# Kernel tuning notes

Measured on AMD Instinct MI355X. Metric: run time of the kernel, lower is better.

Reference implementation:

```python
import jax, jax.numpy as jnp
import numpy as np

# Dims / scalars (from init_kwargs: m = int(T/dt), delta = dt, theta_star = threshold)
M = 50000
N = 500
DELTA = 0.001
GLEAK = 1.0
TAUS = 10.0
THETA_STAR = 1.0
SPIKE_PROB = 0.02  # sparse binary spike raster as produced by time2spike


def setup_inputs() -> dict:
    key = jax.random.key(0)
    k1, k2, k3 = jax.random.split(key, 3)
    # binary spike raster [m, n]
    spikes = (jax.random.uniform(k1, (M, N)) < SPIKE_PROB).astype(jnp.float32)
    # synapse weights ~ N(w_mean=0.01, 0.01)
    w = (0.01 + 0.01 * jax.random.normal(k2, (N,))).astype(jnp.float32)
    # reversal potentials: half excitatory (ex=5), half inhibitory (inh=-1), shuffled
    vrev = jnp.where(jax.random.uniform(k3, (N,)) < 0.5, 5.0, -1.0).astype(jnp.float32)
    return {"spikes": spikes, "w": w, "vrev": vrev}


def reference(spikes, w, vrev):
    dtype = spikes.dtype
    decay = jnp.exp(jnp.asarray(-1.0 / TAUS, dtype))

    # _compute_exp: exp_temp[i] = (exp_temp[i-1] + spikes[i-1]) * exp(-1/taus), exp_temp[0] = 0
    def exp_step(carry, s):
        nxt = (carry + s) * decay
        return nxt, nxt

    _, e_tail = jax.lax.scan(exp_step, jnp.zeros((N,), dtype), spikes[:-1])
    exp_temp = jnp.concatenate([jnp.zeros((1, N), dtype), e_tail], axis=0)  # [M, N]

    # Gsyn_pre = |w| * exp_temp ; Isyn_pre = Vrev * |w| * exp_temp.
    # Only their per-timestep sums over synapses enter the vtr recurrence,
    # so contract over n immediately instead of materializing [M, N] products.
    absw = jnp.abs(w)
    g_sum = exp_temp @ absw            # [M] = sum_j Gsyn_pre[i, j]
    i_sum = exp_temp @ (vrev * absw)   # [M] = sum_j Isyn_pre[i, j]
    a = DELTA * (GLEAK + g_sum)        # per-step leak+conductance factor
    b = DELTA * i_sum                  # per-step input drive

    # _computevtr: if vtr[i-1] < theta: vtr[i] = vtr[i-1]*(1 - a[i-1]) + b[i-1]
    # else vtr[i] stays 0 (state reset after threshold crossing), vtr[0] = 0.
    def vtr_step(v, ab):
        ai, bi = ab
        nxt = jnp.where(v < THETA_STAR, v * (1.0 - ai) + bi, jnp.asarray(0.0, dtype))
        return nxt, nxt

    _, v_tail = jax.lax.scan(vtr_step, jnp.asarray(0.0, dtype), (a[:-1], b[:-1]))
    vtr = jnp.concatenate([jnp.zeros((1,), dtype), v_tail])  # [M]
    return vtr
```

## Files before the change

### kernel.cpp

```cpp
#include <hip/hip_runtime.h>
#include <cmath>

namespace {
constexpr int NELEM  = 50000;
constexpr int NSYN   = 500;
constexpr int NQ4    = 125;
constexpr int T      = 1024;
constexpr int SBLK   = 49;
constexpr int SLOTS  = SBLK * T;
constexpr int CMAXC  = (NELEM - 1) >> 6;
constexpr int NCH_PAD = 784;
constexpr int MAXSEG = 4096;
constexpr int NGRP   = NELEM / 8;
constexpr double DELTA_D = 1.0e-3;
constexpr double THETA_D = 1.0;
constexpr float  DECAY_F = 0.90483741803595957311f;
}

struct WS {
    double2 pq[SLOTS];
    double  rarr[SLOTS];
    double  qarr[SLOTS];
    double  eAm[SLOTS], eAg[SLOTS], eAi[SLOTS];
    double  ePl[SLOTS], eQl[SLOTS];
    double  gAm[64], gAg[64], gAi[64];
    double  gPp[64], gPq[64];
    double  gmaxR[1024];
    double  gbndQ[MAXSEG];
    int     gbnd[MAXSEG];
    int     gnseg;
    int     pad;
    float   swv[SLOTS];
    float   iwv[SLOTS];
};

__global__ __launch_bounds__(256) void k_rowdot(
    const float* __restrict__ spikes,
    const float* __restrict__ w,
    const float* __restrict__ vrev,
    float* __restrict__ swv,
    float* __restrict__ iwv)
{
    const int lane = threadIdx.x & 63;
    const int wv   = threadIdx.x >> 6;
    const int rg   = blockIdx.x * 4 + wv;
    if (rg >= NGRP) return;
    const int row0 = rg * 8;

    const float4* __restrict__ w4 = reinterpret_cast<const float4*>(w);
    const float4* __restrict__ r4 = reinterpret_cast<const float4*>(vrev);
    const int j1 = lane;
    const int j2 = lane + 64;
    const bool has2 = (j2 < NQ4);
    float4 a1 = w4[j1], r1 = r4[j1];
    float4 aw1 = make_float4(fabsf(a1.x), fabsf(a1.y), fabsf(a1.z), fabsf(a1.w));
    float4 ar1 = make_float4(aw1.x * r1.x, aw1.y * r1.y, aw1.z * r1.z, aw1.w * r1.w);
    float4 aw2 = make_float4(0.f, 0.f, 0.f, 0.f), ar2 = aw2;
    if (has2) {
        float4 a2 = w4[j2], r2 = r4[j2];
        aw2 = make_float4(fabsf(a2.x), fabsf(a2.y), fabsf(a2.z), fabsf(a2.w));
        ar2 = make_float4(aw2.x * r2.x, aw2.y * r2.y, aw2.z * r2.z, aw2.w * r2.w);
    }

    float4 s1[8], s2[8];
#pragma unroll
    for (int r = 0; r < 8; ++r) {
        const float4* __restrict__ srow =
            reinterpret_cast<const float4*>(spikes + (size_t)(row0 + r) * NSYN);
        s1[r] = srow[j1];
        if (has2) s2[r] = srow[j2];
    }
    float sp[8], ip[8];
#pragma unroll
    for (int r = 0; r < 8; ++r) {
        float a = s1[r].x * aw1.x + s1[r].y * aw1.y + s1[r].z * aw1.z + s1[r].w * aw1.w;
        float b = s1[r].x * ar1.x + s1[r].y * ar1.y + s1[r].z * ar1.z + s1[r].w * ar1.w;
        if (has2) {
            a += s2[r].x * aw2.x + s2[r].y * aw2.y + s2[r].z * aw2.z + s2[r].w * aw2.w;
            b += s2[r].x * ar2.x + s2[r].y * ar2.y + s2[r].z * ar2.z + s2[r].w * ar2.w;
        }
        sp[r] = a; ip[r] = b;
    }
#pragma unroll
    for (int d = 32; d > 0; d >>= 1) {
#pragma unroll
        for (int r = 0; r < 8; ++r) {
            sp[r] += __shfl_xor(sp[r], d);
            ip[r] += __shfl_xor(ip[r], d);
        }
    }
    if (lane == 0) {
        *reinterpret_cast<float4*>(swv + row0)     = make_float4(sp[0], sp[1], sp[2], sp[3]);
        *reinterpret_cast<float4*>(swv + row0 + 4) = make_float4(sp[4], sp[5], sp[6], sp[7]);
        *reinterpret_cast<float4*>(iwv + row0)     = make_float4(ip[0], ip[1], ip[2], ip[3]);
        *reinterpret_cast<float4*>(iwv + row0 + 4) = make_float4(ip[4], ip[5], ip[6], ip[7]);
    }
}

__global__ __launch_bounds__(1024) void k_scanA(WS* __restrict__ ws)
{
    const int tid = threadIdx.x, lane = tid & 63, wv = tid >> 6, blk = blockIdx.x;
    const int idx = blk * T + tid;
    const bool live = (idx < NELEM);
    const double decay = (double)DECAY_F;
    __shared__ double s_a[16], s_b[16], s_c[16];

    double s = live ? (double)ws->swv[idx] : 0.0;
    double t = live ? (double)ws->iwv[idx] : 0.0;
    double m_in = live ? decay : 1.0;
    double g_in = live ? s * decay : 0.0;
    double i_in = live ? t * decay : 0.0;
#pragma unroll
    for (int d = 1; d < 64; d <<= 1) {
        double pm = __shfl_up(m_in, d);
        double pg = __shfl_up(g_in, d);
        double pi = __shfl_up(i_in, d);
        if (lane >= d) {
            g_in = m_in * pg + g_in;
            i_in = m_in * pi + i_in;
            m_in = pm * m_in;
        }
    }
    if (lane == 63) { s_a[wv] = m_in; s_b[wv] = g_in; s_c[wv] = i_in; }
    __syncthreads();
    if (wv == 0) {
        double wm = (lane < 16) ? s_a[lane] : 1.0;
        double wg = (lane < 16) ? s_b[lane] : 0.0;
        double wi = (lane < 16) ? s_c[lane] : 0.0;
#pragma unroll
        for (int d = 1; d < 16; d <<= 1) {
            double pm = __shfl_up(wm, d);
            double pg = __shfl_up(wg, d);
            double pi = __shfl_up(wi, d);
            if (lane >= d) {
                wg = wm * pg + wg;
                wi = wm * pi + wi;
                wm = pm * wm;
            }
        }
        if (lane < 16) { s_a[lane] = wm; s_b[lane] = wg; s_c[lane] = wi; }
        if (lane == 15) { ws->gAm[blk] = wm; ws->gAg[blk] = wg; ws->gAi[blk] = wi; }
    }
    __syncthreads();
    double em = __shfl_up(m_in, 1), eg = __shfl_up(g_in, 1), ei = __shfl_up(i_in, 1);
    if (lane == 0) { em = 1.0; eg = 0.0; ei = 0.0; }
    if (wv > 0) {
        double qm = s_a[wv - 1], qg = s_b[wv - 1], qi = s_c[wv - 1];
        eg = em * qg + eg;
        ei = em * qi + ei;
        em = qm * em;
    }
    ws->eAm[idx] = em; ws->eAg[idx] = eg; ws->eAi[idx] = ei;
}

__global__ __launch_bounds__(1024) void k_scanB(WS* __restrict__ ws)
{
    const int tid = threadIdx.x, lane = tid & 63, wv = tid >> 6, blk = blockIdx.x;
    const int idx = blk * T + tid;
    const bool live = (idx < NELEM);
    __shared__ double s_a[16], s_b[16];
    __shared__ double s_e[2];

    if (wv == 0) {
        double am = (lane < SBLK) ? ws->gAm[lane] : 1.0;
        double ag = (lane < SBLK) ? ws->gAg[lane] : 0.0;
        double ai = (lane < SBLK) ? ws->gAi[lane] : 0.0;
#pragma unroll
        for (int d = 1; d < 64; d <<= 1) {
            double pm = __shfl_up(am, d);
            double pg = __shfl_up(ag, d);
            double pi = __shfl_up(ai, d);
            if (lane >= d) {
                ag = am * pg + ag;
                ai = am * pi + ai;
                am = pm * am;
            }
        }
        if (blk == 0) {
            if (lane == 0) { s_e[0] = 0.0; s_e[1] = 0.0; }
        } else if (lane == blk - 1) {
            s_e[0] = ag; s_e[1] = ai;
        }
    }
    __syncthreads();

    double em = ws->eAm[idx], eg = ws->eAg[idx], ei = ws->eAi[idx];
    double Eg = em * s_e[0] + eg;
    double Ei = em * s_e[1] + ei;

    double p_in = 1.0, q_in = 0.0;
    if (live) {
        double aa = DELTA_D * (1.0 + Eg);
        double om = 1.0 - aa;
        p_in = om;
        q_in = (DELTA_D * Ei) / om;
    }
#pragma unroll
    for (int d = 1; d < 64; d <<= 1) {
        double pp = __shfl_up(p_in, d);
        double pq = __shfl_up(q_in, d);
        if (lane >= d) {
            q_in = pq + q_in / pp;
            p_in = pp * p_in;
        }
    }
    if (lane == 63) { s_a[wv] = p_in; s_b[wv] = q_in; }
    __syncthreads();
    if (wv == 0) {
        double wp = (lane < 16) ? s_a[lane] : 1.0;
        double wq = (lane < 16) ? s_b[lane] : 0.0;
#pragma unroll
        for (int d = 1; d < 16; d <<= 1) {
            double pp = __shfl_up(wp, d);
            double pq = __shfl_up(wq, d);
            if (lane >= d) {
                wq = pq + wq / pp;
                wp = pp * wp;
            }
        }
        if (lane < 16) { s_a[lane] = wp; s_b[lane] = wq; }
        if (lane == 15) { ws->gPp[blk] = wp; ws->gPq[blk] = wq; }
    }
    __syncthreads();
    double ep = __shfl_up(p_in, 1), eq = __shfl_up(q_in, 1);
    if (lane == 0) { ep = 1.0; eq = 0.0; }
    if (wv > 0) {
        double ap = s_a[wv - 1], aq = s_b[wv - 1];
        eq = aq + eq / ap;
        ep = ap * ep;
    }
    ws->ePl[idx] = ep; ws->eQl[idx] = eq;
}

__global__ __launch_bounds__(1024) void k_apply(WS* __restrict__ ws)
{
    const int tid = threadIdx.x, lane = tid & 63, blk = blockIdx.x;
    const int idx = blk * T + tid;
    const bool live = (idx < NELEM);
    __shared__ double s_e[2];

    if (tid < 64) {
        double ap = (lane < SBLK) ? ws->gPp[lane] : 1.0;
        double aq = (lane < SBLK) ? ws->gPq[lane] : 0.0;
#pragma unroll
        for (int d = 1; d < 64; d <<= 1) {
            double pp = __shfl_up(ap, d);
            double pq = __shfl_up(aq, d);
            if (lane >= d) {
                aq = pq + aq / pp;
                ap = pp * ap;
            }
        }
        if (blk == 0) {
            if (lane == 0) { s_e[0] = 1.0; s_e[1] = 0.0; }
        } else if (lane == blk - 1) {
            s_e[0] = ap; s_e[1] = aq;
        }
    }
    __syncthreads();

    double pl = ws->ePl[idx], ql = ws->eQl[idx];
    double ap = s_e[0], aq = s_e[1];
    double Q = aq + ql / ap;
    double P = ap * pl;
    ws->pq[idx]   = make_double2(P, Q);
    ws->qarr[idx] = Q;
    double R = live ? (Q - THETA_D / P) : -1.0e308;
    ws->rarr[idx] = R;
    double mR = R;
#pragma unroll
    for (int d = 32; d > 0; d >>= 1) mR = fmax(mR, __shfl_xor(mR, d));
    if (lane == 0) ws->gmaxR[idx >> 6] = mR;
}

__global__ __launch_bounds__(1024) void k_search(WS* __restrict__ ws)
{
    const int tid = threadIdx.x;
    __shared__ double smax[NCH_PAD];

    for (int c = tid; c < NCH_PAD; c += T)
        smax[c] = (c <= CMAXC) ? ws->gmaxR[c] : -1.0e308;
    double acc = 0.0;
    for (int i = tid; i < NELEM; i += T) acc += ws->rarr[i];
    for (int i = tid; i < NELEM; i += T) acc += ws->qarr[i];
    if (acc == -1.2345e300) ws->pad = 1;
    __syncthreads();

    if (tid < 64) {
        const int lane = tid;
        int nseg = 1;
        if (lane == 0) { ws->gbnd[0] = 0; ws->gbndQ[0] = 0.0; }
        double Qr = 0.0;
        int pos = 1;
        while (pos < NELEM && nseg < MAXSEG) {
            int c = pos >> 6;
            int i0 = -1;
            while (true) {
                int cf = -1;
                for (int cb = c; cb <= CMAXC; cb += 64) {
                    int cc = cb + lane;
                    bool qy = (cc <= CMAXC) && (smax[cc] >= Qr);
                    unsigned long long m = __ballot(qy);
                    if (m) { cf = cb + __builtin_ctzll(m); break; }
                }
                if (cf < 0) break;
                int i = (cf << 6) + lane;
                bool valid = (i >= pos) && (i < NELEM);
                double rv = valid ? ws->rarr[i] : -1.0e308;
                unsigned long long m2 = __ballot(valid && (rv >= Qr));
                if (m2) { i0 = (cf << 6) + __builtin_ctzll(m2); break; }
                c = cf + 1;
                if (c > CMAXC) break;
            }
            if (i0 < 0) break;
            int nb = i0 + 1;
            if (nb >= NELEM) break;
            Qr = ws->qarr[nb];
            if (lane == 0) { ws->gbnd[nseg] = nb; ws->gbndQ[nseg] = Qr; }
            nseg++;
            pos = nb + 1;
        }
        if (lane == 0) ws->gnseg = nseg;
    }
}

__global__ __launch_bounds__(1024) void k_fill(const WS* __restrict__ ws,
                                               float* __restrict__ out)
{
    __shared__ int    sb[MAXSEG];
    __shared__ double sq[MAXSEG];
    __shared__ int    s_nseg;
    const int tid = threadIdx.x;
    if (tid == 0) s_nseg = ws->gnseg;
    __syncthreads();
    const int nseg = s_nseg;
    for (int i = tid; i < nseg; i += T) { sb[i] = ws->gbnd[i]; sq[i] = ws->gbndQ[i]; }
    __syncthreads();

    const int idx = blockIdx.x * T + tid;
    if (idx < NELEM) {
        int lo = 0, hi = nseg - 1;
        while (lo < hi) {
            int mid = (lo + hi + 1) >> 1;
            if (sb[mid] <= idx) lo = mid; else hi = mid - 1;
        }
        if (idx == sb[lo]) {
            out[idx] = 0.0f;
        } else {
            double2 pl = ws->pq[idx];
            out[idx] = (float)(pl.x * (pl.y - sq[lo]));
        }
    }
}

extern "C" void kernel_launch(void* const* d_in, const int* in_sizes, int n_in,
                              void* d_out, int out_size, void* d_ws, size_t ws_size,
                              hipStream_t stream) {
    const float* spikes = (const float*)d_in[0];
    const float* w      = (const float*)d_in[1];
    const float* vrev   = (const float*)d_in[2];
    float* out = (float*)d_out;
    WS* ws = (WS*)d_ws;

    hipLaunchKernelGGL(k_rowdot, dim3((NGRP + 3) / 4), dim3(256), 0, stream,
                       spikes, w, vrev, ws->swv, ws->iwv);
    hipLaunchKernelGGL(k_scanA,  dim3(SBLK), dim3(T), 0, stream, ws);
    hipLaunchKernelGGL(k_scanB,  dim3(SBLK), dim3(T), 0, stream, ws);
    hipLaunchKernelGGL(k_apply,  dim3(SBLK), dim3(T), 0, stream, ws);
    hipLaunchKernelGGL(k_search, dim3(1),    dim3(T), 0, stream, ws);
    hipLaunchKernelGGL(k_fill,   dim3(SBLK), dim3(T), 0, stream, ws, out);
}
```

Baseline: 215.4 us.

## Fuse threshold search into apply kernel via last-block atomic counter

Merges the single-block segment search into the apply kernel: each block bumps an agent-scope atomic counter after a threadfence, and the last block to finish runs the serial search. This removes one kernel launch and its gap. It also drops the redundant qarr array, reading Q from the pq pairs instead, and removes a dummy full-array read loop in the old search kernel. The counter is reset in the first kernel, which relies on stream ordering. The search now runs inside a 1024-thread block that also did apply work.

```diff
diff --git a/kernel.cpp b/kernel.cpp
--- a/kernel.cpp
+++ b/kernel.cpp
@@ -20,7 +20,6 @@
 struct WS {
     double2 pq[SLOTS];
     double  rarr[SLOTS];
-    double  qarr[SLOTS];
     double  eAm[SLOTS], eAg[SLOTS], eAi[SLOTS];
     double  ePl[SLOTS], eQl[SLOTS];
     double  gAm[64], gAg[64], gAi[64];
@@ -29,7 +28,7 @@
     double  gbndQ[MAXSEG];
     int     gbnd[MAXSEG];
     int     gnseg;
-    int     pad;
+    int     ctr;
     float   swv[SLOTS];
     float   iwv[SLOTS];
 };
@@ -38,9 +37,10 @@
     const float* __restrict__ spikes,
     const float* __restrict__ w,
     const float* __restrict__ vrev,
-    float* __restrict__ swv,
-    float* __restrict__ iwv)
-{
+    WS* __restrict__ ws)
+{
+    if (blockIdx.x == 0 && threadIdx.x == 0) ws->ctr = 0;
+
     const int lane = threadIdx.x & 63;
     const int wv   = threadIdx.x >> 6;
     const int rg   = blockIdx.x * 4 + wv;
@@ -90,10 +90,10 @@
         }
     }
     if (lane == 0) {
-        *reinterpret_cast<float4*>(swv + row0)     = make_float4(sp[0], sp[1], sp[2], sp[3]);
-        *reinterpret_cast<float4*>(swv + row0 + 4) = make_float4(sp[4], sp[5], sp[6], sp[7]);
-        *reinterpret_cast<float4*>(iwv + row0)     = make_float4(ip[0], ip[1], ip[2], ip[3]);
-        *reinterpret_cast<float4*>(iwv + row0 + 4) = make_float4(ip[4], ip[5], ip[6], ip[7]);
+        *reinterpret_cast<float4*>(ws->swv + row0)     = make_float4(sp[0], sp[1], sp[2], sp[3]);
+        *reinterpret_cast<float4*>(ws->swv + row0 + 4) = make_float4(sp[4], sp[5], sp[6], sp[7]);
+        *reinterpret_cast<float4*>(ws->iwv + row0)     = make_float4(ip[0], ip[1], ip[2], ip[3]);
+        *reinterpret_cast<float4*>(ws->iwv + row0 + 4) = make_float4(ip[4], ip[5], ip[6], ip[7]);
     }
 }
 
@@ -232,7 +232,7 @@
     ws->ePl[idx] = ep; ws->eQl[idx] = eq;
 }
 
-__global__ __launch_bounds__(1024) void k_apply(WS* __restrict__ ws)
+__global__ __launch_bounds__(1024) void k_applyS(WS* __restrict__ ws)
 {
     const int tid = threadIdx.x, lane = tid & 63, blk = blockIdx.x;
     const int idx = blk * T + tid;
@@ -263,31 +263,30 @@
     double ap = s_e[0], aq = s_e[1];
     double Q = aq + ql / ap;
     double P = ap * pl;
-    ws->pq[idx]   = make_double2(P, Q);
-    ws->qarr[idx] = Q;
+    ws->pq[idx] = make_double2(P, Q);
     double R = live ? (Q - THETA_D / P) : -1.0e308;
     ws->rarr[idx] = R;
     double mR = R;
 #pragma unroll
     for (int d = 32; d > 0; d >>= 1) mR = fmax(mR, __shfl_xor(mR, d));
     if (lane == 0) ws->gmaxR[idx >> 6] = mR;
-}
-
-__global__ __launch_bounds__(1024) void k_search(WS* __restrict__ ws)
-{
-    const int tid = threadIdx.x;
+
+    __threadfence();
+    __shared__ int s_last;
+    if (tid == 0) {
+        int old = __hip_atomic_fetch_add(&ws->ctr, 1, __ATOMIC_ACQ_REL,
+                                         __HIP_MEMORY_SCOPE_AGENT);
+        s_last = (old == SBLK - 1);
+    }
+    __syncthreads();
+    if (!s_last) return;
+
     __shared__ double smax[NCH_PAD];
-
     for (int c = tid; c < NCH_PAD; c += T)
         smax[c] = (c <= CMAXC) ? ws->gmaxR[c] : -1.0e308;
-    double acc = 0.0;
-    for (int i = tid; i < NELEM; i += T) acc += ws->rarr[i];
-    for (int i = tid; i < NELEM; i += T) acc += ws->qarr[i];
-    if (acc == -1.2345e300) ws->pad = 1;
     __syncthreads();
 
     if (tid < 64) {
-        const int lane = tid;
         int nseg = 1;
         if (lane == 0) { ws->gbnd[0] = 0; ws->gbndQ[0] = 0.0; }
         double Qr = 0.0;
@@ -315,7 +314,7 @@
             if (i0 < 0) break;
             int nb = i0 + 1;
             if (nb >= NELEM) break;
-            Qr = ws->qarr[nb];
+            Qr = ws->pq[nb].y;
             if (lane == 0) { ws->gbnd[nseg] = nb; ws->gbndQ[nseg] = Qr; }
             nseg++;
             pos = nb + 1;
@@ -363,10 +362,9 @@
     WS* ws = (WS*)d_ws;
 
     hipLaunchKernelGGL(k_rowdot, dim3((NGRP + 3) / 4), dim3(256), 0, stream,
-                       spikes, w, vrev, ws->swv, ws->iwv);
+                       spikes, w, vrev, ws);
     hipLaunchKernelGGL(k_scanA,  dim3(SBLK), dim3(T), 0, stream, ws);
     hipLaunchKernelGGL(k_scanB,  dim3(SBLK), dim3(T), 0, stream, ws);
-    hipLaunchKernelGGL(k_apply,  dim3(SBLK), dim3(T), 0, stream, ws);
-    hipLaunchKernelGGL(k_search, dim3(1),    dim3(T), 0, stream, ws);
+    hipLaunchKernelGGL(k_applyS, dim3(SBLK), dim3(T), 0, stream, ws);
     hipLaunchKernelGGL(k_fill,   dim3(SBLK), dim3(T), 0, stream, ws, out);
 }
```

New measurement: 214.7 us. No clear change (-0.3%).
